# Optimization experiments

Measured on AMD Instinct MI355X. Metric: run time of the kernel, lower is better.

Reference implementation:

```python
import jax, jax.numpy as jnp
import numpy as np

N_EMBD = 384
N_HEAD = 6
HEAD_SIZE = N_EMBD // N_HEAD  # 64
B, T = 128, 256
EPS = 1e-5


def setup_inputs() -> dict:
    key = jax.random.key(0)
    ks = jax.random.split(key, 12)
    s = 0.02
    return {
        "x": jax.random.normal(ks[0], (B, T, N_EMBD), dtype=jnp.float32),
        "Wk": jax.random.normal(ks[1], (N_EMBD, N_EMBD), dtype=jnp.float32) * s,
        "Wq": jax.random.normal(ks[2], (N_EMBD, N_EMBD), dtype=jnp.float32) * s,
        "Wv": jax.random.normal(ks[3], (N_EMBD, N_EMBD), dtype=jnp.float32) * s,
        "Wo": jax.random.normal(ks[4], (N_EMBD, N_EMBD), dtype=jnp.float32) * s,
        "bo": jnp.zeros((N_EMBD,), dtype=jnp.float32),
        "W1": jax.random.normal(ks[5], (N_EMBD, 4 * N_EMBD), dtype=jnp.float32) * s,
        "b1": jnp.zeros((4 * N_EMBD,), dtype=jnp.float32),
        "W2": jax.random.normal(ks[6], (4 * N_EMBD, N_EMBD), dtype=jnp.float32) * s,
        "b2": jnp.zeros((N_EMBD,), dtype=jnp.float32),
        "g1": jnp.ones((N_EMBD,), dtype=jnp.float32),
        "be1": jnp.zeros((N_EMBD,), dtype=jnp.float32),
        "g2": jnp.ones((N_EMBD,), dtype=jnp.float32),
        "be2": jnp.zeros((N_EMBD,), dtype=jnp.float32),
    }


def _layernorm(x, g, b):
    mu = jnp.mean(x, axis=-1, keepdims=True)
    var = jnp.var(x, axis=-1, keepdims=True)
    return (x - mu) * jax.lax.rsqrt(var + EPS) * g + b


def _attention(x, Wk, Wq, Wv, Wo, bo):
    Bb, Tt, C = x.shape
    H, D = N_HEAD, HEAD_SIZE
    k = (x @ Wk).reshape(Bb, Tt, H, D).transpose(0, 2, 1, 3)  # (B,H,T,D)
    q = (x @ Wq).reshape(Bb, Tt, H, D).transpose(0, 2, 1, 3)
    v = (x @ Wv).reshape(Bb, Tt, H, D).transpose(0, 2, 1, 3)
    wei = jnp.einsum("bhqd,bhkd->bhqk", q, k) * (D ** -0.5)  # (B,H,T,T)
    mask = jnp.tril(jnp.ones((Tt, Tt), dtype=bool))
    wei = jnp.where(mask, wei, -jnp.inf)
    wei = jax.nn.softmax(wei, axis=-1)
    out = jnp.einsum("bhqk,bhkd->bhqd", wei, v)
    out = out.transpose(0, 2, 1, 3).reshape(Bb, Tt, H * D)
    return out @ Wo + bo


def reference(x, Wk, Wq, Wv, Wo, bo, W1, b1, W2, b2, g1, be1, g2, be2):
    # dropout is identity in eval mode
    h = _layernorm(x, g1, be1)
    x = x + _attention(h, Wk, Wq, Wv, Wo, bo)
    h = _layernorm(x, g2, be2)
    ff = jax.nn.relu(h @ W1 + b1) @ W2 + b2
    return x + ff
```

## Files before the change

### kernel.cpp

```cpp
#include <hip/hip_runtime.h>

typedef unsigned short u16;
typedef short s16x8 __attribute__((ext_vector_type(8)));
typedef float f32x4 __attribute__((ext_vector_type(4)));

__device__ inline u16 f2bf(float f) {
    unsigned u = __float_as_uint(f);
    u += 0x7FFF + ((u >> 16) & 1);
    return (u16)(u >> 16);
}
__device__ inline float bf2f(u16 h) {
    return __uint_as_float((unsigned)h << 16);
}

__device__ inline f32x4 mfma16(s16x8 a, s16x8 b, f32x4 c) {
    return __builtin_amdgcn_mfma_f32_16x16x32_bf16(a, b, c, 0, 0, 0);
}

__device__ __forceinline__ void gl16(const u16* g, u16* l) {
    __builtin_amdgcn_global_load_lds(
        (const __attribute__((address_space(1))) void*)g,
        (__attribute__((address_space(3))) void*)l, 16, 0, 0);
}

__global__ void tcvt_all(const float* __restrict__ Wq, const float* __restrict__ Wk,
                         const float* __restrict__ Wv, const float* __restrict__ Wo,
                         const float* __restrict__ W1, const float* __restrict__ W2,
                         u16* __restrict__ out) {
    int i = blockIdx.x * 256 + threadIdx.x;
    float val;
    if (i < 589824) {
        int q = i / 147456, j = i - q * 147456;
        const float* s = q == 0 ? Wq : q == 1 ? Wk : q == 2 ? Wv : Wo;
        int n = j / 384, k = j - n * 384;
        val = s[k * 384 + n];
    } else if (i < 1179648) {
        int j = i - 589824;
        int n = j / 384, k = j - n * 384;
        val = W1[(size_t)k * 1536 + n];
    } else {
        int j = i - 1179648;
        int n = j / 1536, k = j - n * 1536;
        val = W2[(size_t)k * 384 + n];
    }
    out[i] = f2bf(val);
}

__global__ __launch_bounds__(256) void ln_kernel(const float* __restrict__ x,
                                                 const float* __restrict__ g,
                                                 const float* __restrict__ be,
                                                 u16* __restrict__ out) {
    int lane = threadIdx.x & 63;
    int w = threadIdx.x >> 6;
    int row = blockIdx.x * 4 + w;
    const float* xr = x + (size_t)row * 384;
    float v[6];
    float s = 0.f, sq = 0.f;
#pragma unroll
    for (int i = 0; i < 6; ++i) {
        v[i] = xr[i * 64 + lane];
        s += v[i];
        sq += v[i] * v[i];
    }
#pragma unroll
    for (int m = 1; m < 64; m <<= 1) {
        s += __shfl_xor(s, m);
        sq += __shfl_xor(sq, m);
    }
    float mu = s * (1.0f / 384.0f);
    float var = sq * (1.0f / 384.0f) - mu * mu;
    float rstd = rsqrtf(var + 1e-5f);
    u16* orow = out + (size_t)row * 384;
#pragma unroll
    for (int i = 0; i < 6; ++i) {
        int col = i * 64 + lane;
        orow[col] = f2bf((v[i] - mu) * rstd * g[col] + be[col]);
    }
}

__global__ __launch_bounds__(256) void ln_bf16_kernel(const u16* __restrict__ x,
                                                      const float* __restrict__ g,
                                                      const float* __restrict__ be,
                                                      u16* __restrict__ out) {
    int lane = threadIdx.x & 63;
    int w = threadIdx.x >> 6;
    int row = blockIdx.x * 4 + w;
    const u16* xr = x + (size_t)row * 384;
    bool act = lane < 48;
    float v[8];
    float s = 0.f, sq = 0.f;
    if (act) {
        s16x8 t = *(const s16x8*)&xr[lane * 8];
#pragma unroll
        for (int j = 0; j < 8; ++j) {
            v[j] = bf2f((u16)t[j]);
            s += v[j];
            sq += v[j] * v[j];
        }
    }
#pragma unroll
    for (int m = 1; m < 64; m <<= 1) {
        s += __shfl_xor(s, m);
        sq += __shfl_xor(sq, m);
    }
    float mu = s * (1.0f / 384.0f);
    float var = sq * (1.0f / 384.0f) - mu * mu;
    float rstd = rsqrtf(var + 1e-5f);
    if (act) {
        float4 g0 = *(const float4*)&g[lane * 8];
        float4 g1 = *(const float4*)&g[lane * 8 + 4];
        float4 b0 = *(const float4*)&be[lane * 8];
        float4 b1 = *(const float4*)&be[lane * 8 + 4];
        float gg[8] = {g0.x, g0.y, g0.z, g0.w, g1.x, g1.y, g1.z, g1.w};
        float bb[8] = {b0.x, b0.y, b0.z, b0.w, b1.x, b1.y, b1.z, b1.w};
        u16* orow = out + (size_t)row * 384 + lane * 8;
#pragma unroll
        for (int j = 0; j < 8; ++j)
            orow[j] = f2bf((v[j] - mu) * rstd * gg[j] + bb[j]);
    }
}

template <int BIAS, int RELU, int RES, int RESBF, int OBF16, int NBN>
__global__ __launch_bounds__(512, 4) void gemm_kernel(const u16* __restrict__ A,
                                                      const u16* __restrict__ Bt,
                                                      const float* __restrict__ bias,
                                                      const void* __restrict__ res,
                                                      void* __restrict__ out,
                                                      int M, int N, int K) {
    __shared__ u16 La[2][256 * 32];
    __shared__ u16 Lb[2][128 * 32];
    int tid = threadIdx.x;
    int lane = tid & 63, w = tid >> 6;
    int wm = w >> 1, wn = w & 1;
    int lr = lane & 15, lg = lane >> 4;

    int nwg = gridDim.x;
    int q = nwg >> 3, r = nwg & 7;
    int xcd = blockIdx.x & 7, lin = blockIdx.x >> 3;
    int wg = (xcd < r ? xcd * (q + 1) : r * (q + 1) + (xcd - r) * q) + lin;
    int bx = wg % NBN, by = wg / NBN;
    int m0 = by * 256, n0 = bx * 128;

    int rsub = lane >> 2;
    int gslot = ((lane & 3) ^ ((lane >> 3) & 3)) * 8;
    const u16* pa[2];
    const u16* pb1;
#pragma unroll
    for (int i = 0; i < 2; ++i)
        pa[i] = A + (size_t)(m0 + w * 32 + i * 16 + rsub) * K + gslot;
    pb1 = Bt + (size_t)(n0 + w * 16 + rsub) * K + gslot;

    f32x4 acc[4][4];
    f32x4 zero = {0.f, 0.f, 0.f, 0.f};
#pragma unroll
    for (int mt = 0; mt < 4; ++mt)
#pragma unroll
        for (int nt = 0; nt < 4; ++nt) acc[mt][nt] = zero;

    int sel = (lg ^ ((lr >> 1) & 3)) << 3;
    int nt_steps = K >> 5;

#define STAGE(t, bsel)                                  \
    do {                                                \
        int kc = (t) << 5;                              \
        gl16(pa[0] + kc, &La[bsel][(w * 32) * 32]);     \
        gl16(pa[1] + kc, &La[bsel][(w * 32 + 16) * 32]);\
        gl16(pb1 + kc, &Lb[bsel][(w * 16) * 32]);       \
    } while (0)

    STAGE(0, 0);

    for (int t = 0; t < nt_steps; ++t) {
        asm volatile("s_waitcnt vmcnt(0)" ::: "memory");
        __builtin_amdgcn_s_barrier();
        asm volatile("" ::: "memory");
        if (t + 1 < nt_steps) STAGE(t + 1, (t + 1) & 1);
        const u16* lab = La[t & 1];
        const u16* lbb = Lb[t & 1];
        s16x8 af[4], bfr[4];
#pragma unroll
        for (int mt = 0; mt < 4; ++mt)
            af[mt] = *(const s16x8*)&lab[(wm * 64 + mt * 16 + lr) * 32 + sel];
#pragma unroll
        for (int nt = 0; nt < 4; ++nt)
            bfr[nt] = *(const s16x8*)&lbb[(wn * 64 + nt * 16 + lr) * 32 + sel];
        __builtin_amdgcn_s_setprio(1);
#pragma unroll
        for (int mt = 0; mt < 4; ++mt)
#pragma unroll
            for (int nt = 0; nt < 4; ++nt)
                acc[mt][nt] = mfma16(af[mt], bfr[nt], acc[mt][nt]);
        __builtin_amdgcn_s_setprio(0);
    }
#undef STAGE

#pragma unroll
    for (int mt = 0; mt < 4; ++mt) {
#pragma unroll
        for (int nt = 0; nt < 4; ++nt) {
            int m_base = m0 + wm * 64 + mt * 16 + lg * 4;
            int n = n0 + wn * 64 + nt * 16 + lr;
            float bv = BIAS ? bias[n] : 0.0f;
#pragma unroll
            for (int r2 = 0; r2 < 4; ++r2) {
                size_t idx = (size_t)(m_base + r2) * N + n;
                float val = acc[mt][nt][r2] + bv;
                if (RES) {
                    if (RESBF)
                        val += bf2f(((const u16*)res)[idx]);
                    else
                        val += ((const float*)res)[idx];
                }
                if (RELU) val = fmaxf(val, 0.0f);
                if (OBF16)
                    ((u16*)out)[idx] = f2bf(val);
                else
                    ((float*)out)[idx] = val;
            }
        }
    }
}

__global__ __launch_bounds__(512) void attn_kernel(const u16* __restrict__ qkv,
                                                   u16* __restrict__ aout) {
    __shared__ u16 Kl[256 * 72];
    __shared__ u16 Vt[64 * 264];
    __shared__ u16 Pl[8 * 16 * 264];
    int qt = blockIdx.x, h = blockIdx.y, b = blockIdx.z;
    int tid = threadIdx.x, lane = tid & 63, w = tid >> 6;
    int lr = lane & 15, lg = lane >> 4;
    const u16* qb = qkv + (size_t)b * 256 * 1152;

#pragma unroll
    for (int i = 0; i < 4; ++i) {
        int c = tid + i * 512;
        int t = c >> 3, dch = c & 7;
        *(int4*)&Kl[t * 72 + dch * 8] =
            *(const int4*)(qb + (size_t)t * 1152 + 384 + h * 64 + dch * 8);
        union { int4 v; u16 u[8]; } vv;
        vv.v = *(const int4*)(qb + (size_t)t * 1152 + 768 + h * 64 + dch * 8);
#pragma unroll
        for (int j = 0; j < 8; ++j) Vt[(dch * 8 + j) * 264 + t] = vv.u[j];
    }

    int q0 = qt * 128;
    const u16* qrow = qb + (size_t)(q0 + w * 16 + lr) * 1152 + h * 64;
    s16x8 qf0 = *(const s16x8*)(qrow + lg * 8);
    s16x8 qf1 = *(const s16x8*)(qrow + 32 + lg * 8);

    __syncthreads();

    f32x4 zero = {0.f, 0.f, 0.f, 0.f};
    f32x4 s[16];
#pragma unroll
    for (int nt = 0; nt < 16; ++nt) s[nt] = zero;
#pragma unroll
    for (int nt = 0; nt < 16; ++nt) {
        s16x8 kf0 = *(const s16x8*)&Kl[(nt * 16 + lr) * 72 + lg * 8];
        s16x8 kf1 = *(const s16x8*)&Kl[(nt * 16 + lr) * 72 + 32 + lg * 8];
        s[nt] = mfma16(qf0, kf0, s[nt]);
        s[nt] = mfma16(qf1, kf1, s[nt]);
    }

    int ib = q0 + w * 16 + lg * 4;
    float mx[4] = {-1e30f, -1e30f, -1e30f, -1e30f};
#pragma unroll
    for (int nt = 0; nt < 16; ++nt) {
        int jg = nt * 16 + lr;
#pragma unroll
        for (int r = 0; r < 4; ++r) {
            float val = s[nt][r] * 0.125f;
            val = (jg <= ib + r) ? val : -1e30f;
            s[nt][r] = val;
            mx[r] = fmaxf(mx[r], val);
        }
    }
#pragma unroll
    for (int r = 0; r < 4; ++r) {
        mx[r] = fmaxf(mx[r], __shfl_xor(mx[r], 1));
        mx[r] = fmaxf(mx[r], __shfl_xor(mx[r], 2));
        mx[r] = fmaxf(mx[r], __shfl_xor(mx[r], 4));
        mx[r] = fmaxf(mx[r], __shfl_xor(mx[r], 8));
    }
    float rs[4] = {0.f, 0.f, 0.f, 0.f};
#pragma unroll
    for (int nt = 0; nt < 16; ++nt) {
#pragma unroll
        for (int r = 0; r < 4; ++r) {
            float p = __expf(s[nt][r] - mx[r]);
            s[nt][r] = p;
            rs[r] += p;
        }
    }
#pragma unroll
    for (int r = 0; r < 4; ++r) {
        rs[r] += __shfl_xor(rs[r], 1);
        rs[r] += __shfl_xor(rs[r], 2);
        rs[r] += __shfl_xor(rs[r], 4);
        rs[r] += __shfl_xor(rs[r], 8);
    }
    u16* Pw = &Pl[w * 16 * 264];
#pragma unroll
    for (int nt = 0; nt < 16; ++nt)
#pragma unroll
        for (int r = 0; r < 4; ++r)
            Pw[(lg * 4 + r) * 264 + nt * 16 + lr] = f2bf(s[nt][r]);

    __syncthreads();

    f32x4 o[4];
#pragma unroll
    for (int nt = 0; nt < 4; ++nt) o[nt] = zero;
#pragma unroll
    for (int kc = 0; kc < 8; ++kc) {
        s16x8 pf = *(const s16x8*)&Pw[lr * 264 + kc * 32 + lg * 8];
#pragma unroll
        for (int nt = 0; nt < 4; ++nt) {
            s16x8 vf = *(const s16x8*)&Vt[(nt * 16 + lr) * 264 + kc * 32 + lg * 8];
            o[nt] = mfma16(pf, vf, o[nt]);
        }
    }
    float inv[4];
#pragma unroll
    for (int r = 0; r < 4; ++r) inv[r] = 1.0f / rs[r];
    u16* ob = aout + (size_t)(b * 256 + q0 + w * 16) * 384 + h * 64;
#pragma unroll
    for (int nt = 0; nt < 4; ++nt)
#pragma unroll
        for (int r = 0; r < 4; ++r)
            ob[(size_t)(lg * 4 + r) * 384 + nt * 16 + lr] = f2bf(o[nt][r] * inv[r]);
}

extern "C" void kernel_launch(void* const* d_in, const int* in_sizes, int n_in,
                              void* d_out, int out_size, void* d_ws, size_t ws_size,
                              hipStream_t stream) {
    const float* x   = (const float*)d_in[0];
    const float* Wk  = (const float*)d_in[1];
    const float* Wq  = (const float*)d_in[2];
    const float* Wv  = (const float*)d_in[3];
    const float* Wo  = (const float*)d_in[4];
    const float* bo  = (const float*)d_in[5];
    const float* W1  = (const float*)d_in[6];
    const float* b1  = (const float*)d_in[7];
    const float* W2  = (const float*)d_in[8];
    const float* b2  = (const float*)d_in[9];
    const float* g1  = (const float*)d_in[10];
    const float* be1 = (const float*)d_in[11];
    const float* g2  = (const float*)d_in[12];
    const float* be2 = (const float*)d_in[13];

    char* ws = (char*)d_ws;
    u16* hbuf = (u16*)(ws + 0);
    u16* qkv  = (u16*)(ws + 25165824);
    u16* ao   = (u16*)(ws + 100663296);
    u16* x1   = (u16*)(ws + 125829120);
    u16* ubuf = (u16*)(ws + 25165824);
    u16* wT   = (u16*)(ws + 150994944);
    u16* wqkvT = wT;
    u16* woT   = wT + 442368;
    u16* w1T   = woT + 147456;
    u16* w2T   = w1T + 589824;

    tcvt_all<<<6912, 256, 0, stream>>>(Wq, Wk, Wv, Wo, W1, W2, wT);

    ln_kernel<<<8192, 256, 0, stream>>>(x, g1, be1, hbuf);
    gemm_kernel<0, 0, 0, 0, 1, 9><<<1152, 512, 0, stream>>>(
        hbuf, wqkvT, nullptr, nullptr, qkv, 32768, 1152, 384);
    attn_kernel<<<dim3(2, 6, 128), 512, 0, stream>>>(qkv, ao);
    gemm_kernel<1, 0, 1, 0, 1, 3><<<384, 512, 0, stream>>>(
        ao, woT, bo, x, x1, 32768, 384, 384);
    ln_bf16_kernel<<<8192, 256, 0, stream>>>(x1, g2, be2, hbuf);
    gemm_kernel<1, 1, 0, 0, 1, 12><<<1536, 512, 0, stream>>>(
        hbuf, w1T, b1, nullptr, ubuf, 32768, 1536, 384);
    gemm_kernel<1, 0, 1, 1, 0, 3><<<384, 512, 0, stream>>>(
        ubuf, w2T, b2, x1, (float*)d_out, 32768, 384, 1536);
}
```

Measured before the change: 263.6 us.

## Triple-buffer GEMM LDS staging and interleave loads with MFMA phases

Moves the GEMM main loop from double to triple LDS buffering, prefetching two k-steps ahead and waiting only on the older loads (vmcnt(3)). Each k-step is split into four MFMA phases separated by barriers, with the global->LDS loads for step t+2 spread between them. The aim is to hide global load latency and interleave memory issue with matrix math. In exchange it uses 50% more LDS, which may lower occupancy at the 4-block launch bound, and adds three extra barriers per k-step.

```diff
diff --git a/kernel.cpp b/kernel.cpp
--- a/kernel.cpp
+++ b/kernel.cpp
@@ -127,8 +127,8 @@
                                                       const void* __restrict__ res,
                                                       void* __restrict__ out,
                                                       int M, int N, int K) {
-    __shared__ u16 La[2][256 * 32];
-    __shared__ u16 Lb[2][128 * 32];
+    __shared__ u16 La[3][256 * 32];
+    __shared__ u16 Lb[3][128 * 32];
     int tid = threadIdx.x;
     int lane = tid & 63, w = tid >> 6;
     int wm = w >> 1, wn = w & 1;
@@ -143,12 +143,9 @@
 
     int rsub = lane >> 2;
     int gslot = ((lane & 3) ^ ((lane >> 3) & 3)) * 8;
-    const u16* pa[2];
-    const u16* pb1;
-#pragma unroll
-    for (int i = 0; i < 2; ++i)
-        pa[i] = A + (size_t)(m0 + w * 32 + i * 16 + rsub) * K + gslot;
-    pb1 = Bt + (size_t)(n0 + w * 16 + rsub) * K + gslot;
+    const u16* pa0 = A + (size_t)(m0 + w * 32 + rsub) * K + gslot;
+    const u16* pa1 = A + (size_t)(m0 + w * 32 + 16 + rsub) * K + gslot;
+    const u16* pb1 = Bt + (size_t)(n0 + w * 16 + rsub) * K + gslot;
 
     f32x4 acc[4][4];
     f32x4 zero = {0.f, 0.f, 0.f, 0.f};
@@ -160,39 +157,70 @@
     int sel = (lg ^ ((lr >> 1) & 3)) << 3;
     int nt_steps = K >> 5;
 
-#define STAGE(t, bsel)                                  \
-    do {                                                \
-        int kc = (t) << 5;                              \
-        gl16(pa[0] + kc, &La[bsel][(w * 32) * 32]);     \
-        gl16(pa[1] + kc, &La[bsel][(w * 32 + 16) * 32]);\
-        gl16(pb1 + kc, &Lb[bsel][(w * 16) * 32]);       \
-    } while (0)
-
-    STAGE(0, 0);
-
+    gl16(pa0, &La[0][(w * 32) * 32]);
+    gl16(pa1, &La[0][(w * 32 + 16) * 32]);
+    gl16(pb1, &Lb[0][(w * 16) * 32]);
+    gl16(pa0 + 32, &La[1][(w * 32) * 32]);
+    gl16(pa1 + 32, &La[1][(w * 32 + 16) * 32]);
+    gl16(pb1 + 32, &Lb[1][(w * 16) * 32]);
+
+    int s = 0, wslot = 2;
     for (int t = 0; t < nt_steps; ++t) {
-        asm volatile("s_waitcnt vmcnt(0)" ::: "memory");
+        if (t + 1 < nt_steps)
+            asm volatile("s_waitcnt vmcnt(3)" ::: "memory");
+        else
+            asm volatile("s_waitcnt vmcnt(0)" ::: "memory");
         __builtin_amdgcn_s_barrier();
         asm volatile("" ::: "memory");
-        if (t + 1 < nt_steps) STAGE(t + 1, (t + 1) & 1);
-        const u16* lab = La[t & 1];
-        const u16* lbb = Lb[t & 1];
-        s16x8 af[4], bfr[4];
-#pragma unroll
-        for (int mt = 0; mt < 4; ++mt)
-            af[mt] = *(const s16x8*)&lab[(wm * 64 + mt * 16 + lr) * 32 + sel];
-#pragma unroll
-        for (int nt = 0; nt < 4; ++nt)
-            bfr[nt] = *(const s16x8*)&lbb[(wn * 64 + nt * 16 + lr) * 32 + sel];
+        const u16* lab = La[s];
+        const u16* lbb = Lb[s];
+        bool st = (t + 2 < nt_steps);
+        int kc2 = (t + 2) << 5;
+        s16x8 bfr0, bfr1, bfr2, bfr3, afv;
+        if (st) gl16(pa0 + kc2, &La[wslot][(w * 32) * 32]);
+        bfr0 = *(const s16x8*)&lbb[(wn * 64 + lr) * 32 + sel];
+        bfr1 = *(const s16x8*)&lbb[(wn * 64 + 16 + lr) * 32 + sel];
+        bfr2 = *(const s16x8*)&lbb[(wn * 64 + 32 + lr) * 32 + sel];
+        bfr3 = *(const s16x8*)&lbb[(wn * 64 + 48 + lr) * 32 + sel];
+        afv = *(const s16x8*)&lab[(wm * 64 + lr) * 32 + sel];
         __builtin_amdgcn_s_setprio(1);
-#pragma unroll
-        for (int mt = 0; mt < 4; ++mt)
-#pragma unroll
-            for (int nt = 0; nt < 4; ++nt)
-                acc[mt][nt] = mfma16(af[mt], bfr[nt], acc[mt][nt]);
+        acc[0][0] = mfma16(afv, bfr0, acc[0][0]);
+        acc[0][1] = mfma16(afv, bfr1, acc[0][1]);
+        acc[0][2] = mfma16(afv, bfr2, acc[0][2]);
+        acc[0][3] = mfma16(afv, bfr3, acc[0][3]);
         __builtin_amdgcn_s_setprio(0);
-    }
-#undef STAGE
+        __builtin_amdgcn_s_barrier();
+        asm volatile("" ::: "memory");
+        if (st) gl16(pa1 + kc2, &La[wslot][(w * 32 + 16) * 32]);
+        afv = *(const s16x8*)&lab[(wm * 64 + 16 + lr) * 32 + sel];
+        __builtin_amdgcn_s_setprio(1);
+        acc[1][0] = mfma16(afv, bfr0, acc[1][0]);
+        acc[1][1] = mfma16(afv, bfr1, acc[1][1]);
+        acc[1][2] = mfma16(afv, bfr2, acc[1][2]);
+        acc[1][3] = mfma16(afv, bfr3, acc[1][3]);
+        __builtin_amdgcn_s_setprio(0);
+        __builtin_amdgcn_s_barrier();
+        asm volatile("" ::: "memory");
+        if (st) gl16(pb1 + kc2, &Lb[wslot][(w * 16) * 32]);
+        afv = *(const s16x8*)&lab[(wm * 64 + 32 + lr) * 32 + sel];
+        __builtin_amdgcn_s_setprio(1);
+        acc[2][0] = mfma16(afv, bfr0, acc[2][0]);
+        acc[2][1] = mfma16(afv, bfr1, acc[2][1]);
+        acc[2][2] = mfma16(afv, bfr2, acc[2][2]);
+        acc[2][3] = mfma16(afv, bfr3, acc[2][3]);
+        __builtin_amdgcn_s_setprio(0);
+        __builtin_amdgcn_s_barrier();
+        asm volatile("" ::: "memory");
+        afv = *(const s16x8*)&lab[(wm * 64 + 48 + lr) * 32 + sel];
+        __builtin_amdgcn_s_setprio(1);
+        acc[3][0] = mfma16(afv, bfr0, acc[3][0]);
+        acc[3][1] = mfma16(afv, bfr1, acc[3][1]);
+        acc[3][2] = mfma16(afv, bfr2, acc[3][2]);
+        acc[3][3] = mfma16(afv, bfr3, acc[3][3]);
+        __builtin_amdgcn_s_setprio(0);
+        s = s == 2 ? 0 : s + 1;
+        wslot = wslot == 2 ? 0 : wslot + 1;
+    }
 
 #pragma unroll
     for (int mt = 0; mt < 4; ++mt) {
```

After: 306.6 us. +16.3%, slower.

## Use 4-wave GEMM blocks with 128x64 per-wave tiles and vectorized epilogue

Applied to the files above, without the earlier changes.

The GEMM block shrinks from 8 waves to 4 while keeping the same 256x128 block tile, so each wave now computes a 128x64 sub-tile (8x4 MFMA tiles) and issues more global-to-LDS loads per stage. The MFMA operands are swapped so each lane holds four consecutive output columns, which lets the epilogue use vector loads and stores for bias, residual and output. This aims to raise MFMA work per LDS fragment read and cut scalar epilogue memory traffic. In exchange it doubles the accumulator registers per thread, which can lower occupancy, and halves the waves available to hide latency.

```diff
diff --git a/kernel.cpp b/kernel.cpp
--- a/kernel.cpp
+++ b/kernel.cpp
@@ -121,7 +121,7 @@
 }
 
 template <int BIAS, int RELU, int RES, int RESBF, int OBF16, int NBN>
-__global__ __launch_bounds__(512, 4) void gemm_kernel(const u16* __restrict__ A,
+__global__ __launch_bounds__(256, 2) void gemm_kernel(const u16* __restrict__ A,
                                                       const u16* __restrict__ Bt,
                                                       const float* __restrict__ bias,
                                                       const void* __restrict__ res,
@@ -143,29 +143,34 @@
 
     int rsub = lane >> 2;
     int gslot = ((lane & 3) ^ ((lane >> 3) & 3)) * 8;
-    const u16* pa[2];
-    const u16* pb1;
+    const u16* pa[4];
+    const u16* pb[2];
+#pragma unroll
+    for (int i = 0; i < 4; ++i)
+        pa[i] = A + (size_t)(m0 + w * 64 + i * 16 + rsub) * K + gslot;
 #pragma unroll
     for (int i = 0; i < 2; ++i)
-        pa[i] = A + (size_t)(m0 + w * 32 + i * 16 + rsub) * K + gslot;
-    pb1 = Bt + (size_t)(n0 + w * 16 + rsub) * K + gslot;
-
-    f32x4 acc[4][4];
+        pb[i] = Bt + (size_t)(n0 + w * 32 + i * 16 + rsub) * K + gslot;
+
+    f32x4 acc[8][4];
     f32x4 zero = {0.f, 0.f, 0.f, 0.f};
 #pragma unroll
-    for (int mt = 0; mt < 4; ++mt)
+    for (int mt = 0; mt < 8; ++mt)
 #pragma unroll
         for (int nt = 0; nt < 4; ++nt) acc[mt][nt] = zero;
 
     int sel = (lg ^ ((lr >> 1) & 3)) << 3;
     int nt_steps = K >> 5;
 
-#define STAGE(t, bsel)                                  \
-    do {                                                \
-        int kc = (t) << 5;                              \
-        gl16(pa[0] + kc, &La[bsel][(w * 32) * 32]);     \
-        gl16(pa[1] + kc, &La[bsel][(w * 32 + 16) * 32]);\
-        gl16(pb1 + kc, &Lb[bsel][(w * 16) * 32]);       \
+#define STAGE(t, bsel)                                          \
+    do {                                                        \
+        int kc = (t) << 5;                                      \
+        _Pragma("unroll")                                       \
+        for (int i = 0; i < 4; ++i)                             \
+            gl16(pa[i] + kc, &La[bsel][(w * 64 + i * 16) * 32]);\
+        _Pragma("unroll")                                       \
+        for (int i = 0; i < 2; ++i)                             \
+            gl16(pb[i] + kc, &Lb[bsel][(w * 32 + i * 16) * 32]);\
     } while (0)
 
     STAGE(0, 0);
@@ -177,45 +182,58 @@
         if (t + 1 < nt_steps) STAGE(t + 1, (t + 1) & 1);
         const u16* lab = La[t & 1];
         const u16* lbb = Lb[t & 1];
-        s16x8 af[4], bfr[4];
-#pragma unroll
-        for (int mt = 0; mt < 4; ++mt)
-            af[mt] = *(const s16x8*)&lab[(wm * 64 + mt * 16 + lr) * 32 + sel];
+        s16x8 bfr[4];
 #pragma unroll
         for (int nt = 0; nt < 4; ++nt)
             bfr[nt] = *(const s16x8*)&lbb[(wn * 64 + nt * 16 + lr) * 32 + sel];
         __builtin_amdgcn_s_setprio(1);
 #pragma unroll
-        for (int mt = 0; mt < 4; ++mt)
+        for (int mt = 0; mt < 8; ++mt) {
+            s16x8 af = *(const s16x8*)&lab[(wm * 128 + mt * 16 + lr) * 32 + sel];
 #pragma unroll
             for (int nt = 0; nt < 4; ++nt)
-                acc[mt][nt] = mfma16(af[mt], bfr[nt], acc[mt][nt]);
+                acc[mt][nt] = mfma16(bfr[nt], af, acc[mt][nt]);
+        }
         __builtin_amdgcn_s_setprio(0);
     }
 #undef STAGE
 
 #pragma unroll
-    for (int mt = 0; mt < 4; ++mt) {
+    for (int mt = 0; mt < 8; ++mt) {
+        int m = m0 + wm * 128 + mt * 16 + lr;
 #pragma unroll
         for (int nt = 0; nt < 4; ++nt) {
-            int m_base = m0 + wm * 64 + mt * 16 + lg * 4;
-            int n = n0 + wn * 64 + nt * 16 + lr;
-            float bv = BIAS ? bias[n] : 0.0f;
-#pragma unroll
-            for (int r2 = 0; r2 < 4; ++r2) {
-                size_t idx = (size_t)(m_base + r2) * N + n;
-                float val = acc[mt][nt][r2] + bv;
-                if (RES) {
-                    if (RESBF)
-                        val += bf2f(((const u16*)res)[idx]);
-                    else
-                        val += ((const float*)res)[idx];
+            int n = n0 + wn * 64 + nt * 16 + lg * 4;
+            size_t idx = (size_t)m * N + n;
+            float v0 = acc[mt][nt][0], v1 = acc[mt][nt][1];
+            float v2 = acc[mt][nt][2], v3 = acc[mt][nt][3];
+            if (BIAS) {
+                float4 bv = *(const float4*)&bias[n];
+                v0 += bv.x; v1 += bv.y; v2 += bv.z; v3 += bv.w;
+            }
+            if (RES) {
+                if (RESBF) {
+                    union { int2 i; u16 h[4]; } rv;
+                    rv.i = *(const int2*)((const u16*)res + idx);
+                    v0 += bf2f(rv.h[0]); v1 += bf2f(rv.h[1]);
+                    v2 += bf2f(rv.h[2]); v3 += bf2f(rv.h[3]);
+                } else {
+                    float4 rv = *(const float4*)((const float*)res + idx);
+                    v0 += rv.x; v1 += rv.y; v2 += rv.z; v3 += rv.w;
                 }
-                if (RELU) val = fmaxf(val, 0.0f);
-                if (OBF16)
-                    ((u16*)out)[idx] = f2bf(val);
-                else
-                    ((float*)out)[idx] = val;
+            }
+            if (RELU) {
+                v0 = fmaxf(v0, 0.f); v1 = fmaxf(v1, 0.f);
+                v2 = fmaxf(v2, 0.f); v3 = fmaxf(v3, 0.f);
+            }
+            if (OBF16) {
+                union { int2 i; u16 h[4]; } ov;
+                ov.h[0] = f2bf(v0); ov.h[1] = f2bf(v1);
+                ov.h[2] = f2bf(v2); ov.h[3] = f2bf(v3);
+                *(int2*)((u16*)out + idx) = ov.i;
+            } else {
+                float4 ov = {v0, v1, v2, v3};
+                *(float4*)((float*)out + idx) = ov;
             }
         }
     }
@@ -364,14 +382,14 @@
     tcvt_all<<<6912, 256, 0, stream>>>(Wq, Wk, Wv, Wo, W1, W2, wT);
 
     ln_kernel<<<8192, 256, 0, stream>>>(x, g1, be1, hbuf);
-    gemm_kernel<0, 0, 0, 0, 1, 9><<<1152, 512, 0, stream>>>(
+    gemm_kernel<0, 0, 0, 0, 1, 9><<<1152, 256, 0, stream>>>(
         hbuf, wqkvT, nullptr, nullptr, qkv, 32768, 1152, 384);
     attn_kernel<<<dim3(2, 6, 128), 512, 0, stream>>>(qkv, ao);
-    gemm_kernel<1, 0, 1, 0, 1, 3><<<384, 512, 0, stream>>>(
+    gemm_kernel<1, 0, 1, 0, 1, 3><<<384, 256, 0, stream>>>(
         ao, woT, bo, x, x1, 32768, 384, 384);
     ln_bf16_kernel<<<8192, 256, 0, stream>>>(x1, g2, be2, hbuf);
-    gemm_kernel<1, 1, 0, 0, 1, 12><<<1536, 512, 0, stream>>>(
+    gemm_kernel<1, 1, 0, 0, 1, 12><<<1536, 256, 0, stream>>>(
         hbuf, w1T, b1, nullptr, ubuf, 32768, 1536, 384);
-    gemm_kernel<1, 0, 1, 1, 0, 3><<<384, 512, 0, stream>>>(
+    gemm_kernel<1, 0, 1, 1, 0, 3><<<384, 256, 0, stream>>>(
         ubuf, w2T, b2, x1, (float*)d_out, 32768, 384, 1536);
 }
```

Result: slower. 302.8 us (+14.9%).

## Emit transposed V from QKV GEMM and split attention by causal query tile

Applied to the files above, without the earlier changes.

The QKV GEMM epilogue now writes V directly into a per-(batch, head) transposed layout, so attention can fetch V^T with async global-to-LDS loads into a swizzled buffer. Before, each block transposed V element by element in shared memory. K fragments are now read straight from global memory instead of being staged in LDS. Attention is split into two launches by query tile, so the first tile only computes the 8 causal key blocks and skips the masked half. P is staged in a smaller XOR-swizzled buffer in two halves to cut LDS use and bank conflicts. The cost is scattered 2-byte stores for V^T in the GEMM epilogue, uncached K reads from global, and one extra kernel launch.

```diff
diff --git a/kernel.cpp b/kernel.cpp
--- a/kernel.cpp
+++ b/kernel.cpp
@@ -120,12 +120,13 @@
     }
 }
 
-template <int BIAS, int RELU, int RES, int RESBF, int OBF16, int NBN>
+template <int BIAS, int RELU, int RES, int RESBF, int OBF16, int NBN, int VT>
 __global__ __launch_bounds__(512, 4) void gemm_kernel(const u16* __restrict__ A,
                                                       const u16* __restrict__ Bt,
                                                       const float* __restrict__ bias,
                                                       const void* __restrict__ res,
                                                       void* __restrict__ out,
+                                                      u16* __restrict__ vtout,
                                                       int M, int N, int K) {
     __shared__ u16 La[2][256 * 32];
     __shared__ u16 Lb[2][128 * 32];
@@ -212,52 +213,55 @@
                         val += ((const float*)res)[idx];
                 }
                 if (RELU) val = fmaxf(val, 0.0f);
-                if (OBF16)
+                if (VT && n >= 768) {
+                    int hh = (n - 768) >> 6, dd = (n - 768) & 63;
+                    int m = m_base + r2;
+                    int bb = m >> 8, tt = m & 255;
+                    vtout[((((size_t)bb * 6 + hh) << 6) + dd) * 256 + tt] = f2bf(val);
+                } else if (OBF16) {
                     ((u16*)out)[idx] = f2bf(val);
-                else
+                } else {
                     ((float*)out)[idx] = val;
+                }
             }
         }
     }
 }
 
+template <int QT0>
 __global__ __launch_bounds__(512) void attn_kernel(const u16* __restrict__ qkv,
+                                                   const u16* __restrict__ vt,
                                                    u16* __restrict__ aout) {
-    __shared__ u16 Kl[256 * 72];
-    __shared__ u16 Vt[64 * 264];
-    __shared__ u16 Pl[8 * 16 * 264];
-    int qt = blockIdx.x, h = blockIdx.y, b = blockIdx.z;
+    __shared__ u16 Vt[64 * 256];
+    __shared__ u16 Pl[8][16 * 128];
+    int h = blockIdx.x, b = blockIdx.y;
     int tid = threadIdx.x, lane = tid & 63, w = tid >> 6;
     int lr = lane & 15, lg = lane >> 4;
     const u16* qb = qkv + (size_t)b * 256 * 1152;
+    const u16* vb = vt + (((size_t)b * 6 + h) << 14);
 
 #pragma unroll
     for (int i = 0; i < 4; ++i) {
-        int c = tid + i * 512;
-        int t = c >> 3, dch = c & 7;
-        *(int4*)&Kl[t * 72 + dch * 8] =
-            *(const int4*)(qb + (size_t)t * 1152 + 384 + h * 64 + dch * 8);
-        union { int4 v; u16 u[8]; } vv;
-        vv.v = *(const int4*)(qb + (size_t)t * 1152 + 768 + h * 64 + dch * 8);
-#pragma unroll
-        for (int j = 0; j < 8; ++j) Vt[(dch * 8 + j) * 264 + t] = vv.u[j];
-    }
-
-    int q0 = qt * 128;
+        int d = w * 8 + i * 2 + (lane >> 5);
+        int ss = (lane & 31) ^ (d & 31);
+        gl16(vb + d * 256 + ss * 8, &Vt[(w * 8 + i * 2) * 256]);
+    }
+
+    const int q0 = QT0 ? 0 : 128;
+    const int NT = QT0 ? 8 : 16;
     const u16* qrow = qb + (size_t)(q0 + w * 16 + lr) * 1152 + h * 64;
     s16x8 qf0 = *(const s16x8*)(qrow + lg * 8);
     s16x8 qf1 = *(const s16x8*)(qrow + 32 + lg * 8);
 
-    __syncthreads();
-
     f32x4 zero = {0.f, 0.f, 0.f, 0.f};
-    f32x4 s[16];
-#pragma unroll
-    for (int nt = 0; nt < 16; ++nt) s[nt] = zero;
-#pragma unroll
-    for (int nt = 0; nt < 16; ++nt) {
-        s16x8 kf0 = *(const s16x8*)&Kl[(nt * 16 + lr) * 72 + lg * 8];
-        s16x8 kf1 = *(const s16x8*)&Kl[(nt * 16 + lr) * 72 + 32 + lg * 8];
+    f32x4 s[NT];
+#pragma unroll
+    for (int nt = 0; nt < NT; ++nt) s[nt] = zero;
+#pragma unroll
+    for (int nt = 0; nt < NT; ++nt) {
+        const u16* krow = qb + (size_t)(nt * 16 + lr) * 1152 + 384 + h * 64;
+        s16x8 kf0 = *(const s16x8*)(krow + lg * 8);
+        s16x8 kf1 = *(const s16x8*)(krow + 32 + lg * 8);
         s[nt] = mfma16(qf0, kf0, s[nt]);
         s[nt] = mfma16(qf1, kf1, s[nt]);
     }
@@ -265,7 +269,7 @@
     int ib = q0 + w * 16 + lg * 4;
     float mx[4] = {-1e30f, -1e30f, -1e30f, -1e30f};
 #pragma unroll
-    for (int nt = 0; nt < 16; ++nt) {
+    for (int nt = 0; nt < NT; ++nt) {
         int jg = nt * 16 + lr;
 #pragma unroll
         for (int r = 0; r < 4; ++r) {
@@ -284,7 +288,7 @@
     }
     float rs[4] = {0.f, 0.f, 0.f, 0.f};
 #pragma unroll
-    for (int nt = 0; nt < 16; ++nt) {
+    for (int nt = 0; nt < NT; ++nt) {
 #pragma unroll
         for (int r = 0; r < 4; ++r) {
             float p = __expf(s[nt][r] - mx[r]);
@@ -299,27 +303,59 @@
         rs[r] += __shfl_xor(rs[r], 4);
         rs[r] += __shfl_xor(rs[r], 8);
     }
-    u16* Pw = &Pl[w * 16 * 264];
-#pragma unroll
-    for (int nt = 0; nt < 16; ++nt)
-#pragma unroll
-        for (int r = 0; r < 4; ++r)
-            Pw[(lg * 4 + r) * 264 + nt * 16 + lr] = f2bf(s[nt][r]);
-
-    __syncthreads();
-
+
+    asm volatile("s_waitcnt vmcnt(0)" ::: "memory");
+    __builtin_amdgcn_s_barrier();
+    asm volatile("" ::: "memory");
+
+    u16* Pw = Pl[w];
     f32x4 o[4];
 #pragma unroll
     for (int nt = 0; nt < 4; ++nt) o[nt] = zero;
-#pragma unroll
-    for (int kc = 0; kc < 8; ++kc) {
-        s16x8 pf = *(const s16x8*)&Pw[lr * 264 + kc * 32 + lg * 8];
+
+#pragma unroll
+    for (int nt = 0; nt < 8; ++nt) {
+        int col = nt * 16 + lr;
+        int phys = (col >> 3) ^ (lg * 4);
+#pragma unroll
+        for (int r = 0; r < 4; ++r) {
+            int row = lg * 4 + r;
+            Pw[row * 128 + ((col >> 3) ^ row) * 8 + (col & 7)] = f2bf(s[nt][r]);
+        }
+        (void)phys;
+    }
+#pragma unroll
+    for (int kc = 0; kc < 4; ++kc) {
+        s16x8 pf = *(const s16x8*)&Pw[lr * 128 + ((kc * 4 + lg) ^ lr) * 8];
 #pragma unroll
         for (int nt = 0; nt < 4; ++nt) {
-            s16x8 vf = *(const s16x8*)&Vt[(nt * 16 + lr) * 264 + kc * 32 + lg * 8];
+            int row = nt * 16 + lr;
+            s16x8 vf = *(const s16x8*)&Vt[row * 256 + ((kc * 4 + lg) ^ (row & 31)) * 8];
             o[nt] = mfma16(pf, vf, o[nt]);
         }
     }
+    if (!QT0) {
+#pragma unroll
+        for (int nt = 8; nt < 16; ++nt) {
+            int col = (nt - 8) * 16 + lr;
+#pragma unroll
+            for (int r = 0; r < 4; ++r) {
+                int row = lg * 4 + r;
+                Pw[row * 128 + ((col >> 3) ^ row) * 8 + (col & 7)] = f2bf(s[nt][r]);
+            }
+        }
+#pragma unroll
+        for (int kc = 4; kc < 8; ++kc) {
+            s16x8 pf = *(const s16x8*)&Pw[lr * 128 + (((kc - 4) * 4 + lg) ^ lr) * 8];
+#pragma unroll
+            for (int nt = 0; nt < 4; ++nt) {
+                int row = nt * 16 + lr;
+                s16x8 vf = *(const s16x8*)&Vt[row * 256 + ((kc * 4 + lg) ^ (row & 31)) * 8];
+                o[nt] = mfma16(pf, vf, o[nt]);
+            }
+        }
+    }
+
     float inv[4];
 #pragma unroll
     for (int r = 0; r < 4; ++r) inv[r] = 1.0f / rs[r];
@@ -356,6 +392,7 @@
     u16* x1   = (u16*)(ws + 125829120);
     u16* ubuf = (u16*)(ws + 25165824);
     u16* wT   = (u16*)(ws + 150994944);
+    u16* vt   = (u16*)(ws + 154533888);
     u16* wqkvT = wT;
     u16* woT   = wT + 442368;
     u16* w1T   = woT + 147456;
@@ -364,14 +401,15 @@
     tcvt_all<<<6912, 256, 0, stream>>>(Wq, Wk, Wv, Wo, W1, W2, wT);
 
     ln_kernel<<<8192, 256, 0, stream>>>(x, g1, be1, hbuf);
-    gemm_kernel<0, 0, 0, 0, 1, 9><<<1152, 512, 0, stream>>>(
-        hbuf, wqkvT, nullptr, nullptr, qkv, 32768, 1152, 384);
-    attn_kernel<<<dim3(2, 6, 128), 512, 0, stream>>>(qkv, ao);
-    gemm_kernel<1, 0, 1, 0, 1, 3><<<384, 512, 0, stream>>>(
-        ao, woT, bo, x, x1, 32768, 384, 384);
+    gemm_kernel<0, 0, 0, 0, 1, 9, 1><<<1152, 512, 0, stream>>>(
+        hbuf, wqkvT, nullptr, nullptr, qkv, vt, 32768, 1152, 384);
+    attn_kernel<1><<<dim3(6, 128), 512, 0, stream>>>(qkv, vt, ao);
+    attn_kernel<0><<<dim3(6, 128), 512, 0, stream>>>(qkv, vt, ao);
+    gemm_kernel<1, 0, 1, 0, 1, 3, 0><<<384, 512, 0, stream>>>(
+        ao, woT, bo, x, x1, nullptr, 32768, 384, 384);
     ln_bf16_kernel<<<8192, 256, 0, stream>>>(x1, g2, be2, hbuf);
-    gemm_kernel<1, 1, 0, 0, 1, 12><<<1536, 512, 0, stream>>>(
-        hbuf, w1T, b1, nullptr, ubuf, 32768, 1536, 384);
-    gemm_kernel<1, 0, 1, 1, 0, 3><<<384, 512, 0, stream>>>(
-        ubuf, w2T, b2, x1, (float*)d_out, 32768, 384, 1536);
-}
+    gemm_kernel<1, 1, 0, 0, 1, 12, 0><<<1536, 512, 0, stream>>>(
+        hbuf, w1T, b1, nullptr, ubuf, nullptr, 32768, 1536, 384);
+    gemm_kernel<1, 0, 1, 1, 0, 3, 0><<<384, 512, 0, stream>>>(
+        ubuf, w2T, b2, x1, (float*)d_out, nullptr, 32768, 384, 1536);
+}
```

After: 302.6 us. 1.15x slower.
